# Kernel optimization log

Hardware: AMD Instinct MI355X
Metric: run time of the kernel (lower is better)

Reference implementation:

```python
import jax, jax.numpy as jnp
import numpy as np

N_NODES = 50000
N_EDGES = 800000
N_GRAPHS = 512
EPS = 1e-5
SLOPE = 0.2  # LeakyReLU negative slope in GATv2


def setup_inputs() -> dict:
    key = jax.random.key(0)
    ks = jax.random.split(key, 20)
    s = 0.1
    inp = {
        "x": jax.random.normal(ks[0], (N_NODES, 9), jnp.float32),
        "edge_attr": jax.random.normal(ks[1], (N_EDGES, 3), jnp.float32),
        "Wl0": jax.random.normal(ks[2], (9, 64), jnp.float32) * s,
        "Wr0": jax.random.normal(ks[3], (9, 64), jnp.float32) * s,
        "bl0": jnp.zeros((64,), jnp.float32),
        "br0": jnp.zeros((64,), jnp.float32),
        "We0": jax.random.normal(ks[4], (3, 64), jnp.float32) * s,
        "att0": jax.random.normal(ks[5], (64,), jnp.float32) * s,
        "bo0": jnp.zeros((64,), jnp.float32),
        "Wl": jax.random.normal(ks[6], (4, 64, 64), jnp.float32) * s,
        "Wr": jax.random.normal(ks[7], (4, 64, 64), jnp.float32) * s,
        "bl": jnp.zeros((4, 64), jnp.float32),
        "br": jnp.zeros((4, 64), jnp.float32),
        "We": jax.random.normal(ks[8], (4, 3, 64), jnp.float32) * s,
        "att": jax.random.normal(ks[9], (4, 64), jnp.float32) * s,
        "bo": jnp.zeros((4, 64), jnp.float32),
        "bn_g": jnp.ones((5, 64), jnp.float32),
        "bn_b": jnp.zeros((5, 64), jnp.float32),
        "bn_m": jnp.zeros((5, 64), jnp.float32),
        "bn_v": jax.random.uniform(ks[10], (5, 64), jnp.float32, 0.5, 1.5),
        "Wjk": jax.random.normal(ks[11], (64, 64), jnp.float32) * s,
        "bjk": jnp.zeros((64,), jnp.float32),
        "Whead": jax.random.normal(ks[12], (64, 1), jnp.float32) * s,
        "bhead": jnp.zeros((1,), jnp.float32),
        "edge_index": jax.random.randint(ks[13], (2, N_EDGES), 0, N_NODES, jnp.int32),
        "batch": jnp.sort(jax.random.randint(ks[14], (N_NODES,), 0, N_GRAPHS, jnp.int32)),
        "num_graphs": N_GRAPHS,
    }
    return inp


def gatv2_layer(h, src, dst, ea, Wl_, bl_, Wr_, br_, We_, a_, bo_, n_nodes):
    # GATv2Conv (heads=1, edge_dim) : e_ij = a . LeakyReLU(Wl h_j + Wr h_i + We e_ij)
    xl = h @ Wl_ + bl_                          # [N, 64] source transform
    xr = h @ Wr_ + br_                          # [N, 64] dest transform
    e = jax.nn.leaky_relu(xl[src] + xr[dst] + ea @ We_, SLOPE)  # [E, 64]
    logit = e @ a_                              # [E]
    m = jax.ops.segment_max(logit, dst, num_segments=n_nodes)
    m = jnp.where(jnp.isfinite(m), m, 0.0)      # empty segments -> -inf
    p = jnp.exp(logit - m[dst])
    z = jax.ops.segment_sum(p, dst, num_segments=n_nodes)
    alpha = p / jnp.maximum(z[dst], 1e-16)      # softmax over in-edges of dst
    out = jax.ops.segment_sum(alpha[:, None] * xl[src], dst, num_segments=n_nodes)
    return out + bo_


def bn_relu(h, g, b, m, v):
    # eval-mode BatchNorm1d followed by ReLU (BasicGNN: norm then act)
    return jax.nn.relu((h - m) * (g * jax.lax.rsqrt(v + EPS)) + b)


def reference(x, edge_attr, Wl0, Wr0, bl0, br0, We0, att0, bo0,
              Wl, Wr, bl, br, We, att, bo,
              bn_g, bn_b, bn_m, bn_v, Wjk, bjk, Whead, bhead,
              edge_index, batch, num_graphs):
    n = x.shape[0]
    src, dst = edge_index[0], edge_index[1]
    h = gatv2_layer(x, src, dst, edge_attr, Wl0, bl0, Wr0, br0, We0, att0, bo0, n)
    h = bn_relu(h, bn_g[0], bn_b[0], bn_m[0], bn_v[0])
    for i in range(4):
        h = gatv2_layer(h, src, dst, edge_attr, Wl[i], bl[i], Wr[i], br[i], We[i], att[i], bo[i], n)
        h = bn_relu(h, bn_g[i + 1], bn_b[i + 1], bn_m[i + 1], bn_v[i + 1])
    h = h @ Wjk + bjk                            # jk='last' output projection 64->64
    # global mean pool over graphs
    sums = jax.ops.segment_sum(h, batch, num_segments=num_graphs)          # [G, 64]
    cnt = jax.ops.segment_sum(jnp.ones((n,), h.dtype), batch, num_segments=num_graphs)
    pooled = sums / jnp.maximum(cnt, 1.0)[:, None]
    return pooled @ Whead + bhead                # [G, 1]  (dropout inactive in eval)
```

## Files before the change

### kernel.cpp

```cpp
#include <hip/hip_runtime.h>
#include <math.h>

#define N_NODES 50000
#define N_EDGES 800000
#define N_GRAPHS 512
#define SLOPE 0.2f
#define CAP 48
static constexpr float EPS_BN = 1e-5f;

typedef float v2f __attribute__((ext_vector_type(2)));


__global__ __launch_bounds__(256) void scatter_t9_kernel(
    const int* __restrict__ src, const int* __restrict__ dst,
    const float* __restrict__ ea,
    int* __restrict__ cnt, float4* __restrict__ rec,
    const float* __restrict__ x,
    const float* __restrict__ Wl0, const float* __restrict__ bl0,
    const float* __restrict__ Wr0, const float* __restrict__ br0,
    float* __restrict__ xl, float* __restrict__ xr) {
    int t = threadIdx.x;
    int e = blockIdx.x * 256 + t;
    if (e < N_EDGES) {
        int d = dst[e];
        int pos = atomicAdd(&cnt[d], 1);
        if (pos < CAP)
            rec[(size_t)d * CAP + pos] = make_float4(__int_as_float(src[e] * 64),
                                                     ea[e * 3 + 0], ea[e * 3 + 1], ea[e * 3 + 2]);
    }

    int w = t >> 6;
    int k = t & 63;
    v2f wlr[9];
#pragma unroll
    for (int j = 0; j < 9; j++) wlr[j] = (v2f){Wl0[j * 64 + k], Wr0[j * 64 + k]};
    v2f bias = {bl0[k], br0[k]};
    const int NW = gridDim.x * 4;
    for (int n = blockIdx.x * 4 + w; n < N_NODES; n += NW) {
        int un = __builtin_amdgcn_readfirstlane(n);
        const float* __restrict__ hrow = x + (size_t)un * 9;
        float hb[9];
#pragma unroll
        for (int j = 0; j < 9; j++) hb[j] = hrow[j];
        v2f acc = bias;
#pragma unroll
        for (int j = 0; j < 9; j++)
            acc = __builtin_elementwise_fma((v2f){hb[j], hb[j]}, wlr[j], acc);
        xl[(size_t)un * 64 + k] = acc.x;
        xr[(size_t)un * 64 + k] = acc.y;
    }
}


__global__ __launch_bounds__(256) void transform5_kernel(
    const float* __restrict__ h,
    const float* __restrict__ Wl, const float* __restrict__ bl,
    const float* __restrict__ Wr, const float* __restrict__ br,
    float* __restrict__ xl, float* __restrict__ xr) {
    __shared__ float sAt[64][68];
    __shared__ float sB[64][128];
    int t = threadIdx.x;
    int n0 = blockIdx.x * 64;

#pragma unroll
    for (int i = 0; i < 4; i++) {
        int idx = i * 256 + t;
        int row = idx >> 4;
        int fc  = idx & 15;
        int n = n0 + row;
        float4 v = (n < N_NODES) ? *((const float4*)(h + (size_t)n * 64 + fc * 4))
                                 : make_float4(0.f, 0.f, 0.f, 0.f);
        sAt[fc * 4 + 0][row] = v.x;
        sAt[fc * 4 + 1][row] = v.y;
        sAt[fc * 4 + 2][row] = v.z;
        sAt[fc * 4 + 3][row] = v.w;
    }
#pragma unroll
    for (int i = 0; i < 8; i++) {
        int idx = i * 256 + t;
        int j  = idx >> 5;
        int fc = idx & 31;
        int c  = fc * 4;
        float4 v = (c < 64) ? *((const float4*)(Wl + j * 64 + c))
                            : *((const float4*)(Wr + j * 64 + (c - 64)));
        *((float4*)&sB[j][c]) = v;
    }
    __syncthreads();

    int tx = t & 15, ty = t >> 4;
    int col0 = tx * 8;
    const float* bsrc = (col0 < 64) ? (bl + col0) : (br + (col0 - 64));
    v2f acc[4][4];
#pragma unroll
    for (int r = 0; r < 4; r++)
#pragma unroll
        for (int cc = 0; cc < 4; cc++)
            acc[r][cc] = (v2f){bsrc[cc * 2], bsrc[cc * 2 + 1]};

#pragma unroll 4
    for (int j = 0; j < 64; j++) {
        float a0 = sAt[j][ty * 4 + 0];
        float a1 = sAt[j][ty * 4 + 1];
        float a2 = sAt[j][ty * 4 + 2];
        float a3 = sAt[j][ty * 4 + 3];
        float4 bq0 = *((const float4*)&sB[j][col0]);
        float4 bq1 = *((const float4*)&sB[j][col0 + 4]);
        v2f b0 = {bq0.x, bq0.y}, b1 = {bq0.z, bq0.w};
        v2f b2 = {bq1.x, bq1.y}, b3 = {bq1.z, bq1.w};
        v2f a0v = {a0, a0}, a1v = {a1, a1}, a2v = {a2, a2}, a3v = {a3, a3};
        acc[0][0] = __builtin_elementwise_fma(a0v, b0, acc[0][0]);
        acc[0][1] = __builtin_elementwise_fma(a0v, b1, acc[0][1]);
        acc[0][2] = __builtin_elementwise_fma(a0v, b2, acc[0][2]);
        acc[0][3] = __builtin_elementwise_fma(a0v, b3, acc[0][3]);
        acc[1][0] = __builtin_elementwise_fma(a1v, b0, acc[1][0]);
        acc[1][1] = __builtin_elementwise_fma(a1v, b1, acc[1][1]);
        acc[1][2] = __builtin_elementwise_fma(a1v, b2, acc[1][2]);
        acc[1][3] = __builtin_elementwise_fma(a1v, b3, acc[1][3]);
        acc[2][0] = __builtin_elementwise_fma(a2v, b0, acc[2][0]);
        acc[2][1] = __builtin_elementwise_fma(a2v, b1, acc[2][1]);
        acc[2][2] = __builtin_elementwise_fma(a2v, b2, acc[2][2]);
        acc[2][3] = __builtin_elementwise_fma(a2v, b3, acc[2][3]);
        acc[3][0] = __builtin_elementwise_fma(a3v, b0, acc[3][0]);
        acc[3][1] = __builtin_elementwise_fma(a3v, b1, acc[3][1]);
        acc[3][2] = __builtin_elementwise_fma(a3v, b2, acc[3][2]);
        acc[3][3] = __builtin_elementwise_fma(a3v, b3, acc[3][3]);
    }

#pragma unroll
    for (int r = 0; r < 4; r++) {
        int n = n0 + ty * 4 + r;
        if (n < N_NODES) {
            float4 lo = make_float4(acc[r][0].x, acc[r][0].y, acc[r][1].x, acc[r][1].y);
            float4 hi = make_float4(acc[r][2].x, acc[r][2].y, acc[r][3].x, acc[r][3].y);
            float* dstp = (col0 < 64) ? (xl + (size_t)n * 64 + col0)
                                      : (xr + (size_t)n * 64 + (col0 - 64));
            *((float4*)dstp) = lo;
            *((float4*)(dstp + 4)) = hi;
        }
    }
}


__global__ __launch_bounds__(256) void gat_fused7_kernel(
    const float* __restrict__ xl, const float* __restrict__ xr,
    const float4* __restrict__ recP, const int* __restrict__ cnt,
    const float* __restrict__ We, const float* __restrict__ att,
    const float* __restrict__ bo,
    const float* __restrict__ bn_g, const float* __restrict__ bn_b,
    const float* __restrict__ bn_m, const float* __restrict__ bn_v,
    float* __restrict__ hout) {
    int t = threadIdx.x;
    int w = t >> 6;
    int lane = t & 63;
    int q = lane >> 4;
    int r = lane & 15;
    int k4 = r * 4;
    int n = blockIdx.x * 4 + w;

    float4 we0 = *(const float4*)(We + 0 * 64 + k4);
    float4 we1 = *(const float4*)(We + 64 + k4);
    float4 we2 = *(const float4*)(We + 128 + k4);
    float4 at4 = *(const float4*)(att + k4);
    float4 xq  = *(const float4*)(xr + (size_t)n * 64 + k4);
    v2f we0a = {we0.x, we0.y}, we0b = {we0.z, we0.w};
    v2f we1a = {we1.x, we1.y}, we1b = {we1.z, we1.w};
    v2f we2a = {we2.x, we2.y}, we2b = {we2.z, we2.w};
    v2f ata  = {at4.x, at4.y}, atb  = {at4.z, at4.w};
    v2f xra  = {xq.x, xq.y},   xrb  = {xq.z, xq.w};
    int beg = n * CAP;
    int end = beg + min(cnt[n], CAP);

    v2f oAa = {0.f, 0.f}, oAb = {0.f, 0.f};
    v2f oBa = {0.f, 0.f}, oBb = {0.f, 0.f};
    float zA = 0.f, zB = 0.f;

    for (int c = beg; c < end; c += 8) {
        int pA = c + q;     bool vA = pA < end; int iA = vA ? pA : beg;
        int pB = c + 4 + q; bool vB = pB < end; int iB = vB ? pB : beg;
        float4 rA = recP[iA];
        float4 rB = recP[iB];
        unsigned offA = (unsigned)__float_as_int(rA.x) + k4;
        unsigned offB = (unsigned)__float_as_int(rB.x) + k4;
        float4 xA = *(const float4*)(xl + offA);
        float4 xB = *(const float4*)(xl + offB);
        v2f xAa = {xA.x, xA.y}, xAb = {xA.z, xA.w};
        v2f xBa = {xB.x, xB.y}, xBb = {xB.z, xB.w};

        v2f tAa = xAa + xra, tAb = xAb + xrb;
        v2f tBa = xBa + xra, tBb = xBb + xrb;
        tAa = __builtin_elementwise_fma((v2f){rA.y, rA.y}, we0a, tAa);
        tAb = __builtin_elementwise_fma((v2f){rA.y, rA.y}, we0b, tAb);
        tBa = __builtin_elementwise_fma((v2f){rB.y, rB.y}, we0a, tBa);
        tBb = __builtin_elementwise_fma((v2f){rB.y, rB.y}, we0b, tBb);
        tAa = __builtin_elementwise_fma((v2f){rA.z, rA.z}, we1a, tAa);
        tAb = __builtin_elementwise_fma((v2f){rA.z, rA.z}, we1b, tAb);
        tBa = __builtin_elementwise_fma((v2f){rB.z, rB.z}, we1a, tBa);
        tBb = __builtin_elementwise_fma((v2f){rB.z, rB.z}, we1b, tBb);
        tAa = __builtin_elementwise_fma((v2f){rA.w, rA.w}, we2a, tAa);
        tAb = __builtin_elementwise_fma((v2f){rA.w, rA.w}, we2b, tAb);
        tBa = __builtin_elementwise_fma((v2f){rB.w, rB.w}, we2a, tBa);
        tBb = __builtin_elementwise_fma((v2f){rB.w, rB.w}, we2b, tBb);

        tAa = __builtin_elementwise_max(tAa, tAa * SLOPE);
        tAb = __builtin_elementwise_max(tAb, tAb * SLOPE);
        tBa = __builtin_elementwise_max(tBa, tBa * SLOPE);
        tBb = __builtin_elementwise_max(tBb, tBb * SLOPE);

        v2f dA = ata * tAa; dA = __builtin_elementwise_fma(atb, tAb, dA);
        v2f dB = ata * tBa; dB = __builtin_elementwise_fma(atb, tBb, dB);
        float accA = dA.x + dA.y;
        float accB = dB.x + dB.y;

        accA += __shfl_xor(accA, 1, 64);  accB += __shfl_xor(accB, 1, 64);
        accA += __shfl_xor(accA, 2, 64);  accB += __shfl_xor(accB, 2, 64);
        accA += __shfl_xor(accA, 4, 64);  accB += __shfl_xor(accB, 4, 64);
        accA += __shfl_xor(accA, 8, 64);  accB += __shfl_xor(accB, 8, 64);

        float peA = vA ? __expf(accA) : 0.f;
        float peB = vB ? __expf(accB) : 0.f;
        v2f pA2 = {peA, peA}, pB2 = {peB, peB};
        oAa = __builtin_elementwise_fma(pA2, xAa, oAa);
        oAb = __builtin_elementwise_fma(pA2, xAb, oAb);
        oBa = __builtin_elementwise_fma(pB2, xBa, oBa);
        oBb = __builtin_elementwise_fma(pB2, xBb, oBb);
        zA += peA; zB += peB;
    }

    v2f oa = oAa + oBa, ob = oAb + oBb;
    float z = zA + zB;
    float4 o = make_float4(oa.x, oa.y, ob.x, ob.y);
    o.x += __shfl_xor(o.x, 16, 64); o.x += __shfl_xor(o.x, 32, 64);
    o.y += __shfl_xor(o.y, 16, 64); o.y += __shfl_xor(o.y, 32, 64);
    o.z += __shfl_xor(o.z, 16, 64); o.z += __shfl_xor(o.z, 32, 64);
    o.w += __shfl_xor(o.w, 16, 64); o.w += __shfl_xor(o.w, 32, 64);
    z += __shfl_xor(z, 16, 64); z += __shfl_xor(z, 32, 64);

    if (q == 0) {
        float zi = 1.0f / fmaxf(z, 1e-16f);
        float4 bo4 = *(const float4*)(bo + k4);
        float4 g4  = *(const float4*)(bn_g + k4);
        float4 b4  = *(const float4*)(bn_b + k4);
        float4 m4  = *(const float4*)(bn_m + k4);
        float4 v4  = *(const float4*)(bn_v + k4);
        float4 res;
        res.x = fmaxf((o.x * zi + bo4.x - m4.x) * (g4.x / sqrtf(v4.x + EPS_BN)) + b4.x, 0.f);
        res.y = fmaxf((o.y * zi + bo4.y - m4.y) * (g4.y / sqrtf(v4.y + EPS_BN)) + b4.y, 0.f);
        res.z = fmaxf((o.z * zi + bo4.z - m4.z) * (g4.z / sqrtf(v4.z + EPS_BN)) + b4.z, 0.f);
        res.w = fmaxf((o.w * zi + bo4.w - m4.w) * (g4.w / sqrtf(v4.w + EPS_BN)) + b4.w, 0.f);
        *(float4*)(hout + (size_t)n * 64 + k4) = res;
    }
}


__global__ __launch_bounds__(64) void pool_all_kernel(
    const float* __restrict__ h, const int* __restrict__ batch,
    const float* __restrict__ Wjk, const float* __restrict__ bjk,
    const float* __restrict__ Whead, const float* __restrict__ bhead,
    float* __restrict__ out) {
    int g = blockIdx.x;
    int k = threadIdx.x;
    int lo = 0, hi = N_NODES;
    while (lo < hi) { int mid = (lo + hi) >> 1; if (batch[mid] < g) lo = mid + 1; else hi = mid; }
    int s = lo;
    hi = N_NODES;
    while (lo < hi) { int mid = (lo + hi) >> 1; if (batch[mid] < g + 1) lo = mid + 1; else hi = mid; }
    int e = lo;

    float wc = 0.f;
    for (int j = 0; j < 64; j++) wc = fmaf(Wjk[k * 64 + j], Whead[j], wc);
    float bc = bjk[k] * Whead[k];
    for (int off = 32; off > 0; off >>= 1) bc += __shfl_xor(bc, off, 64);

    float acc = 0.f;
    for (int n = s; n < e; ++n) acc += h[(size_t)n * 64 + k];
    float cntf = (float)(e - s);
    acc /= fmaxf(cntf, 1.0f);
    float v = acc * wc;
    for (int off = 32; off > 0; off >>= 1) v += __shfl_xor(v, off, 64);
    if (k == 0) out[g] = v + bc + bhead[0];
}


extern "C" void kernel_launch(void* const* d_in, const int* in_sizes, int n_in,
                              void* d_out, int out_size, void* d_ws, size_t ws_size,
                              hipStream_t stream) {
    const float* x     = (const float*)d_in[0];
    const float* ea    = (const float*)d_in[1];
    const float* Wl0   = (const float*)d_in[2];
    const float* Wr0   = (const float*)d_in[3];
    const float* bl0   = (const float*)d_in[4];
    const float* br0   = (const float*)d_in[5];
    const float* We0   = (const float*)d_in[6];
    const float* att0  = (const float*)d_in[7];
    const float* bo0   = (const float*)d_in[8];
    const float* Wl    = (const float*)d_in[9];
    const float* Wr    = (const float*)d_in[10];
    const float* bl    = (const float*)d_in[11];
    const float* br    = (const float*)d_in[12];
    const float* We    = (const float*)d_in[13];
    const float* att   = (const float*)d_in[14];
    const float* bo    = (const float*)d_in[15];
    const float* bn_g  = (const float*)d_in[16];
    const float* bn_b  = (const float*)d_in[17];
    const float* bn_m  = (const float*)d_in[18];
    const float* bn_v  = (const float*)d_in[19];
    const float* Wjk   = (const float*)d_in[20];
    const float* bjk   = (const float*)d_in[21];
    const float* Whead = (const float*)d_in[22];
    const float* bhead = (const float*)d_in[23];
    const int* edge_index = (const int*)d_in[24];
    const int* batch      = (const int*)d_in[25];

    const int* srcIdx = edge_index;
    const int* dstIdx = edge_index + N_EDGES;

    char* ws = (char*)d_ws;
    size_t off = 0;
    auto alloc = [&](size_t bytes) -> void* {
        void* p = ws + off;
        off += (bytes + 255) & ~(size_t)255;
        return p;
    };
    float* hA      = (float*)alloc((size_t)N_NODES * 64 * 4);
    float* hB      = (float*)alloc((size_t)N_NODES * 64 * 4);
    float* xlb     = (float*)alloc((size_t)N_NODES * 64 * 4);
    float* xrb     = (float*)alloc((size_t)N_NODES * 64 * 4);
    int*   cnt     = (int*)alloc((size_t)N_NODES * 4);
    float4* recP   = (float4*)alloc((size_t)N_NODES * CAP * 16);

    hipMemsetAsync(cnt, 0, (size_t)N_NODES * 4, stream);
    scatter_t9_kernel<<<(N_EDGES + 255) / 256, 256, 0, stream>>>(
        srcIdx, dstIdx, ea, cnt, recP, x, Wl0, bl0, Wr0, br0, xlb, xrb);

    const int NBN = N_NODES / 4;
    const int NBG = (N_NODES + 63) / 64;

    gat_fused7_kernel<<<NBN, 256, 0, stream>>>(xlb, xrb, recP, cnt,
                                               We0, att0, bo0,
                                               bn_g, bn_b, bn_m, bn_v, hA);

    float* hcur = hA;
    float* hnext = hB;
    for (int i = 0; i < 4; i++) {
        transform5_kernel<<<NBG, 256, 0, stream>>>(hcur,
            Wl + (size_t)i * 64 * 64, bl + (size_t)i * 64,
            Wr + (size_t)i * 64 * 64, br + (size_t)i * 64,
            xlb, xrb);
        gat_fused7_kernel<<<NBN, 256, 0, stream>>>(xlb, xrb, recP, cnt,
            We + (size_t)i * 3 * 64, att + (size_t)i * 64,
            bo + (size_t)i * 64,
            bn_g + (size_t)(i + 1) * 64, bn_b + (size_t)(i + 1) * 64,
            bn_m + (size_t)(i + 1) * 64, bn_v + (size_t)(i + 1) * 64,
            hnext);
        float* tp = hcur; hcur = hnext; hnext = tp;
    }

    pool_all_kernel<<<N_GRAPHS, 64, 0, stream>>>(hcur, batch, Wjk, bjk, Whead, bhead,
                                                 (float*)d_out);
}
```

Measured before the change: 499.2 us.

## Unroll edge loops, batch scatter loads, and parallelize pooling across waves

The GAT aggregation loop now handles 16 edges per iteration (four independent chains instead of two) so more gathers are in flight, and it gains a 4-block occupancy hint. The scatter kernel gives each thread two edges and issues all loads before the atomics. The transform kernel lays out columns so each thread writes matching xl and xr float4s, and pooling uses four waves per graph with a shared-memory reduction. These trade more registers in the edge loop for latency hiding, and halve the scatter grid, which changes how the fused node-transform loop is spread across blocks.

```diff
diff --git a/kernel.cpp b/kernel.cpp
--- a/kernel.cpp
+++ b/kernel.cpp
@@ -11,7 +11,7 @@
 typedef float v2f __attribute__((ext_vector_type(2)));
 
 
-__global__ __launch_bounds__(256) void scatter_t9_kernel(
+__global__ __launch_bounds__(256) void scatter_t10_kernel(
     const int* __restrict__ src, const int* __restrict__ dst,
     const float* __restrict__ ea,
     int* __restrict__ cnt, float4* __restrict__ rec,
@@ -20,14 +20,24 @@
     const float* __restrict__ Wr0, const float* __restrict__ br0,
     float* __restrict__ xl, float* __restrict__ xr) {
     int t = threadIdx.x;
-    int e = blockIdx.x * 256 + t;
-    if (e < N_EDGES) {
-        int d = dst[e];
-        int pos = atomicAdd(&cnt[d], 1);
-        if (pos < CAP)
-            rec[(size_t)d * CAP + pos] = make_float4(__int_as_float(src[e] * 64),
-                                                     ea[e * 3 + 0], ea[e * 3 + 1], ea[e * 3 + 2]);
-    }
+    int e0 = blockIdx.x * 512 + t;
+    int e1 = e0 + 256;
+    bool v0 = e0 < N_EDGES;
+    bool v1 = e1 < N_EDGES;
+    int ec0 = v0 ? e0 : 0;
+    int ec1 = v1 ? e1 : 0;
+    int d0 = dst[ec0];
+    int d1 = dst[ec1];
+    int s0 = src[ec0];
+    int s1 = src[ec1];
+    float a00 = ea[ec0 * 3 + 0], a01 = ea[ec0 * 3 + 1], a02 = ea[ec0 * 3 + 2];
+    float a10 = ea[ec1 * 3 + 0], a11 = ea[ec1 * 3 + 1], a12 = ea[ec1 * 3 + 2];
+    int p0 = v0 ? atomicAdd(&cnt[d0], 1) : CAP;
+    int p1 = v1 ? atomicAdd(&cnt[d1], 1) : CAP;
+    if (v0 && p0 < CAP)
+        rec[(size_t)d0 * CAP + p0] = make_float4(__int_as_float(s0 * 64), a00, a01, a02);
+    if (v1 && p1 < CAP)
+        rec[(size_t)d1 * CAP + p1] = make_float4(__int_as_float(s1 * 64), a10, a11, a12);
 
     int w = t >> 6;
     int k = t & 63;
@@ -52,7 +62,7 @@
 }
 
 
-__global__ __launch_bounds__(256) void transform5_kernel(
+__global__ __launch_bounds__(256) void transform6_kernel(
     const float* __restrict__ h,
     const float* __restrict__ Wl, const float* __restrict__ bl,
     const float* __restrict__ Wr, const float* __restrict__ br,
@@ -88,14 +98,17 @@
     __syncthreads();
 
     int tx = t & 15, ty = t >> 4;
-    int col0 = tx * 8;
-    const float* bsrc = (col0 < 64) ? (bl + col0) : (br + (col0 - 64));
+    int c0 = tx * 4;
+    float4 bls = *((const float4*)(bl + c0));
+    float4 brs = *((const float4*)(br + c0));
     v2f acc[4][4];
 #pragma unroll
-    for (int r = 0; r < 4; r++)
-#pragma unroll
-        for (int cc = 0; cc < 4; cc++)
-            acc[r][cc] = (v2f){bsrc[cc * 2], bsrc[cc * 2 + 1]};
+    for (int r = 0; r < 4; r++) {
+        acc[r][0] = (v2f){bls.x, bls.y};
+        acc[r][1] = (v2f){bls.z, bls.w};
+        acc[r][2] = (v2f){brs.x, brs.y};
+        acc[r][3] = (v2f){brs.z, brs.w};
+    }
 
 #pragma unroll 4
     for (int j = 0; j < 64; j++) {
@@ -103,8 +116,8 @@
         float a1 = sAt[j][ty * 4 + 1];
         float a2 = sAt[j][ty * 4 + 2];
         float a3 = sAt[j][ty * 4 + 3];
-        float4 bq0 = *((const float4*)&sB[j][col0]);
-        float4 bq1 = *((const float4*)&sB[j][col0 + 4]);
+        float4 bq0 = *((const float4*)&sB[j][c0]);
+        float4 bq1 = *((const float4*)&sB[j][64 + c0]);
         v2f b0 = {bq0.x, bq0.y}, b1 = {bq0.z, bq0.w};
         v2f b2 = {bq1.x, bq1.y}, b3 = {bq1.z, bq1.w};
         v2f a0v = {a0, a0}, a1v = {a1, a1}, a2v = {a2, a2}, a3v = {a3, a3};
@@ -130,18 +143,32 @@
     for (int r = 0; r < 4; r++) {
         int n = n0 + ty * 4 + r;
         if (n < N_NODES) {
-            float4 lo = make_float4(acc[r][0].x, acc[r][0].y, acc[r][1].x, acc[r][1].y);
-            float4 hi = make_float4(acc[r][2].x, acc[r][2].y, acc[r][3].x, acc[r][3].y);
-            float* dstp = (col0 < 64) ? (xl + (size_t)n * 64 + col0)
-                                      : (xr + (size_t)n * 64 + (col0 - 64));
-            *((float4*)dstp) = lo;
-            *((float4*)(dstp + 4)) = hi;
+            *((float4*)(xl + (size_t)n * 64 + c0)) =
+                make_float4(acc[r][0].x, acc[r][0].y, acc[r][1].x, acc[r][1].y);
+            *((float4*)(xr + (size_t)n * 64 + c0)) =
+                make_float4(acc[r][2].x, acc[r][2].y, acc[r][3].x, acc[r][3].y);
         }
     }
 }
 
 
-__global__ __launch_bounds__(256) void gat_fused7_kernel(
+#define EDGE_T(rX, xXa, xXb, accX)                                        \
+    {                                                                     \
+        v2f tXa = xXa + xra, tXb = xXb + xrb;                             \
+        tXa = __builtin_elementwise_fma((v2f){rX.y, rX.y}, we0a, tXa);    \
+        tXb = __builtin_elementwise_fma((v2f){rX.y, rX.y}, we0b, tXb);    \
+        tXa = __builtin_elementwise_fma((v2f){rX.z, rX.z}, we1a, tXa);    \
+        tXb = __builtin_elementwise_fma((v2f){rX.z, rX.z}, we1b, tXb);    \
+        tXa = __builtin_elementwise_fma((v2f){rX.w, rX.w}, we2a, tXa);    \
+        tXb = __builtin_elementwise_fma((v2f){rX.w, rX.w}, we2b, tXb);    \
+        tXa = __builtin_elementwise_max(tXa, tXa * SLOPE);                \
+        tXb = __builtin_elementwise_max(tXb, tXb * SLOPE);                \
+        v2f dX = ata * tXa;                                               \
+        dX = __builtin_elementwise_fma(atb, tXb, dX);                     \
+        accX = dX.x + dX.y;                                               \
+    }
+
+__global__ __launch_bounds__(256, 4) void gat_fused8_kernel(
     const float* __restrict__ xl, const float* __restrict__ xr,
     const float4* __restrict__ recP, const int* __restrict__ cnt,
     const float* __restrict__ We, const float* __restrict__ att,
@@ -172,62 +199,66 @@
 
     v2f oAa = {0.f, 0.f}, oAb = {0.f, 0.f};
     v2f oBa = {0.f, 0.f}, oBb = {0.f, 0.f};
-    float zA = 0.f, zB = 0.f;
-
-    for (int c = beg; c < end; c += 8) {
-        int pA = c + q;     bool vA = pA < end; int iA = vA ? pA : beg;
-        int pB = c + 4 + q; bool vB = pB < end; int iB = vB ? pB : beg;
-        float4 rA = recP[iA];
-        float4 rB = recP[iB];
+    v2f oCa = {0.f, 0.f}, oCb = {0.f, 0.f};
+    v2f oDa = {0.f, 0.f}, oDb = {0.f, 0.f};
+    float zA = 0.f, zB = 0.f, zC = 0.f, zD = 0.f;
+
+    for (int c = beg; c < end; c += 16) {
+        int pA = c + q;      bool vA = pA < end;
+        int pB = c + 4 + q;  bool vB = pB < end;
+        int pC = c + 8 + q;  bool vC = pC < end;
+        int pD = c + 12 + q; bool vD = pD < end;
+        float4 rA = recP[vA ? pA : beg];
+        float4 rB = recP[vB ? pB : beg];
+        float4 rC = recP[vC ? pC : beg];
+        float4 rD = recP[vD ? pD : beg];
         unsigned offA = (unsigned)__float_as_int(rA.x) + k4;
         unsigned offB = (unsigned)__float_as_int(rB.x) + k4;
+        unsigned offC = (unsigned)__float_as_int(rC.x) + k4;
+        unsigned offD = (unsigned)__float_as_int(rD.x) + k4;
         float4 xA = *(const float4*)(xl + offA);
         float4 xB = *(const float4*)(xl + offB);
+        float4 xC = *(const float4*)(xl + offC);
+        float4 xD = *(const float4*)(xl + offD);
         v2f xAa = {xA.x, xA.y}, xAb = {xA.z, xA.w};
         v2f xBa = {xB.x, xB.y}, xBb = {xB.z, xB.w};
-
-        v2f tAa = xAa + xra, tAb = xAb + xrb;
-        v2f tBa = xBa + xra, tBb = xBb + xrb;
-        tAa = __builtin_elementwise_fma((v2f){rA.y, rA.y}, we0a, tAa);
-        tAb = __builtin_elementwise_fma((v2f){rA.y, rA.y}, we0b, tAb);
-        tBa = __builtin_elementwise_fma((v2f){rB.y, rB.y}, we0a, tBa);
-        tBb = __builtin_elementwise_fma((v2f){rB.y, rB.y}, we0b, tBb);
-        tAa = __builtin_elementwise_fma((v2f){rA.z, rA.z}, we1a, tAa);
-        tAb = __builtin_elementwise_fma((v2f){rA.z, rA.z}, we1b, tAb);
-        tBa = __builtin_elementwise_fma((v2f){rB.z, rB.z}, we1a, tBa);
-        tBb = __builtin_elementwise_fma((v2f){rB.z, rB.z}, we1b, tBb);
-        tAa = __builtin_elementwise_fma((v2f){rA.w, rA.w}, we2a, tAa);
-        tAb = __builtin_elementwise_fma((v2f){rA.w, rA.w}, we2b, tAb);
-        tBa = __builtin_elementwise_fma((v2f){rB.w, rB.w}, we2a, tBa);
-        tBb = __builtin_elementwise_fma((v2f){rB.w, rB.w}, we2b, tBb);
-
-        tAa = __builtin_elementwise_max(tAa, tAa * SLOPE);
-        tAb = __builtin_elementwise_max(tAb, tAb * SLOPE);
-        tBa = __builtin_elementwise_max(tBa, tBa * SLOPE);
-        tBb = __builtin_elementwise_max(tBb, tBb * SLOPE);
-
-        v2f dA = ata * tAa; dA = __builtin_elementwise_fma(atb, tAb, dA);
-        v2f dB = ata * tBa; dB = __builtin_elementwise_fma(atb, tBb, dB);
-        float accA = dA.x + dA.y;
-        float accB = dB.x + dB.y;
-
-        accA += __shfl_xor(accA, 1, 64);  accB += __shfl_xor(accB, 1, 64);
-        accA += __shfl_xor(accA, 2, 64);  accB += __shfl_xor(accB, 2, 64);
-        accA += __shfl_xor(accA, 4, 64);  accB += __shfl_xor(accB, 4, 64);
-        accA += __shfl_xor(accA, 8, 64);  accB += __shfl_xor(accB, 8, 64);
+        v2f xCa = {xC.x, xC.y}, xCb = {xC.z, xC.w};
+        v2f xDa = {xD.x, xD.y}, xDb = {xD.z, xD.w};
+
+        float accA, accB, accC, accD;
+        EDGE_T(rA, xAa, xAb, accA);
+        EDGE_T(rB, xBa, xBb, accB);
+        EDGE_T(rC, xCa, xCb, accC);
+        EDGE_T(rD, xDa, xDb, accD);
+
+        accA += __shfl_xor(accA, 1, 64); accB += __shfl_xor(accB, 1, 64);
+        accC += __shfl_xor(accC, 1, 64); accD += __shfl_xor(accD, 1, 64);
+        accA += __shfl_xor(accA, 2, 64); accB += __shfl_xor(accB, 2, 64);
+        accC += __shfl_xor(accC, 2, 64); accD += __shfl_xor(accD, 2, 64);
+        accA += __shfl_xor(accA, 4, 64); accB += __shfl_xor(accB, 4, 64);
+        accC += __shfl_xor(accC, 4, 64); accD += __shfl_xor(accD, 4, 64);
+        accA += __shfl_xor(accA, 8, 64); accB += __shfl_xor(accB, 8, 64);
+        accC += __shfl_xor(accC, 8, 64); accD += __shfl_xor(accD, 8, 64);
 
         float peA = vA ? __expf(accA) : 0.f;
         float peB = vB ? __expf(accB) : 0.f;
-        v2f pA2 = {peA, peA}, pB2 = {peB, peB};
+        float peC = vC ? __expf(accC) : 0.f;
+        float peD = vD ? __expf(accD) : 0.f;
+        v2f pA2 = {peA, peA}, pB2 = {peB, peB}, pC2 = {peC, peC}, pD2 = {peD, peD};
         oAa = __builtin_elementwise_fma(pA2, xAa, oAa);
         oAb = __builtin_elementwise_fma(pA2, xAb, oAb);
         oBa = __builtin_elementwise_fma(pB2, xBa, oBa);
         oBb = __builtin_elementwise_fma(pB2, xBb, oBb);
-        zA += peA; zB += peB;
-    }
-
-    v2f oa = oAa + oBa, ob = oAb + oBb;
-    float z = zA + zB;
+        oCa = __builtin_elementwise_fma(pC2, xCa, oCa);
+        oCb = __builtin_elementwise_fma(pC2, xCb, oCb);
+        oDa = __builtin_elementwise_fma(pD2, xDa, oDa);
+        oDb = __builtin_elementwise_fma(pD2, xDb, oDb);
+        zA += peA; zB += peB; zC += peC; zD += peD;
+    }
+
+    v2f oa = (oAa + oBa) + (oCa + oDa);
+    v2f ob = (oAb + oBb) + (oCb + oDb);
+    float z = (zA + zB) + (zC + zD);
     float4 o = make_float4(oa.x, oa.y, ob.x, ob.y);
     o.x += __shfl_xor(o.x, 16, 64); o.x += __shfl_xor(o.x, 32, 64);
     o.y += __shfl_xor(o.y, 16, 64); o.y += __shfl_xor(o.y, 32, 64);
@@ -252,13 +283,16 @@
 }
 
 
-__global__ __launch_bounds__(64) void pool_all_kernel(
+__global__ __launch_bounds__(256) void pool_all2_kernel(
     const float* __restrict__ h, const int* __restrict__ batch,
     const float* __restrict__ Wjk, const float* __restrict__ bjk,
     const float* __restrict__ Whead, const float* __restrict__ bhead,
     float* __restrict__ out) {
+    __shared__ float red[4][64];
     int g = blockIdx.x;
-    int k = threadIdx.x;
+    int t = threadIdx.x;
+    int k = t & 63;
+    int w = t >> 6;
     int lo = 0, hi = N_NODES;
     while (lo < hi) { int mid = (lo + hi) >> 1; if (batch[mid] < g) lo = mid + 1; else hi = mid; }
     int s = lo;
@@ -266,18 +300,23 @@
     while (lo < hi) { int mid = (lo + hi) >> 1; if (batch[mid] < g + 1) lo = mid + 1; else hi = mid; }
     int e = lo;
 
-    float wc = 0.f;
-    for (int j = 0; j < 64; j++) wc = fmaf(Wjk[k * 64 + j], Whead[j], wc);
-    float bc = bjk[k] * Whead[k];
-    for (int off = 32; off > 0; off >>= 1) bc += __shfl_xor(bc, off, 64);
-
     float acc = 0.f;
-    for (int n = s; n < e; ++n) acc += h[(size_t)n * 64 + k];
-    float cntf = (float)(e - s);
-    acc /= fmaxf(cntf, 1.0f);
-    float v = acc * wc;
-    for (int off = 32; off > 0; off >>= 1) v += __shfl_xor(v, off, 64);
-    if (k == 0) out[g] = v + bc + bhead[0];
+    for (int n = s + w; n < e; n += 4) acc += h[(size_t)n * 64 + k];
+    red[w][k] = acc;
+    __syncthreads();
+
+    if (w == 0) {
+        acc = (red[0][k] + red[1][k]) + (red[2][k] + red[3][k]);
+        float wc = 0.f;
+        for (int j = 0; j < 64; j++) wc = fmaf(Wjk[k * 64 + j], Whead[j], wc);
+        float bc = bjk[k] * Whead[k];
+        for (int off = 32; off > 0; off >>= 1) bc += __shfl_xor(bc, off, 64);
+        float cntf = (float)(e - s);
+        acc /= fmaxf(cntf, 1.0f);
+        float v = acc * wc;
+        for (int off = 32; off > 0; off >>= 1) v += __shfl_xor(v, off, 64);
+        if (k == 0) out[g] = v + bc + bhead[0];
+    }
 }
 
 
@@ -329,24 +368,25 @@
     float4* recP   = (float4*)alloc((size_t)N_NODES * CAP * 16);
 
     hipMemsetAsync(cnt, 0, (size_t)N_NODES * 4, stream);
-    scatter_t9_kernel<<<(N_EDGES + 255) / 256, 256, 0, stream>>>(
+    const int NSB = (N_EDGES + 511) / 512;
+    scatter_t10_kernel<<<NSB, 256, 0, stream>>>(
         srcIdx, dstIdx, ea, cnt, recP, x, Wl0, bl0, Wr0, br0, xlb, xrb);
 
     const int NBN = N_NODES / 4;
     const int NBG = (N_NODES + 63) / 64;
 
-    gat_fused7_kernel<<<NBN, 256, 0, stream>>>(xlb, xrb, recP, cnt,
+    gat_fused8_kernel<<<NBN, 256, 0, stream>>>(xlb, xrb, recP, cnt,
                                                We0, att0, bo0,
                                                bn_g, bn_b, bn_m, bn_v, hA);
 
     float* hcur = hA;
     float* hnext = hB;
     for (int i = 0; i < 4; i++) {
-        transform5_kernel<<<NBG, 256, 0, stream>>>(hcur,
+        transform6_kernel<<<NBG, 256, 0, stream>>>(hcur,
             Wl + (size_t)i * 64 * 64, bl + (size_t)i * 64,
             Wr + (size_t)i * 64 * 64, br + (size_t)i * 64,
             xlb, xrb);
-        gat_fused7_kernel<<<NBN, 256, 0, stream>>>(xlb, xrb, recP, cnt,
+        gat_fused8_kernel<<<NBN, 256, 0, stream>>>(xlb, xrb, recP, cnt,
             We + (size_t)i * 3 * 64, att + (size_t)i * 64,
             bo + (size_t)i * 64,
             bn_g + (size_t)(i + 1) * 64, bn_b + (size_t)(i + 1) * 64,
@@ -355,6 +395,6 @@
         float* tp = hcur; hcur = hnext; hnext = tp;
     }
 
-    pool_all_kernel<<<N_GRAPHS, 64, 0, stream>>>(hcur, batch, Wjk, bjk, Whead, bhead,
-                                                 (float*)d_out);
+    pool_all2_kernel<<<N_GRAPHS, 256, 0, stream>>>(hcur, batch, Wjk, bjk, Whead, bhead,
+                                                   (float*)d_out);
 }
```

New measurement: 518.2 us. +3.8%, slower.
